# Kernel tuning notes

Measured on AMD Instinct MI355X. Metric: run time of the kernel, lower is better.

The kernel has to match this reference:

```python
import jax, jax.numpy as jnp
import numpy as np

NPOINT = 1024
RADII = (0.1, 0.2)
NSAMPLES = (16, 32)
IN_CH = 64
OUT = 256
EPS = 1e-5


def fps(pts, npoint):
    # pts: (N,3) -> (npoint,) int32 farthest-point-sampling indices (starts at index 0)
    N = pts.shape[0]
    def body(carry, _):
        dists, last = carry
        d = jnp.sum((pts - pts[last]) ** 2, axis=-1)
        dists = jnp.minimum(dists, d)
        nxt = jnp.argmax(dists).astype(jnp.int32)
        return (dists, nxt), last
    _, idx = jax.lax.scan(body, (jnp.full((N,), 1e10, pts.dtype), jnp.int32(0)), None, length=npoint)
    return idx


def ball_query(radius, k, xyz, new_xyz):
    # xyz (B,N,3), new_xyz (B,S,3) -> (B,S,k) int32; first k points within radius,
    # padded with the first in-range index (matches pointnet2 ball_query semantics;
    # each centroid is itself a point so at least one index is always in range).
    N = xyz.shape[1]
    d2 = jnp.sum((new_xyz[:, :, None, :] - xyz[:, None, :, :]) ** 2, axis=-1)  # (B,S,N)
    mask = d2 < radius * radius
    key = jnp.where(mask, jnp.arange(N, dtype=jnp.int32)[None, None, :], N)
    order = jnp.argsort(key, axis=-1)[..., :k]            # (B,S,k)
    sel_key = jnp.take_along_axis(key, order, axis=-1)
    valid = sel_key < N
    first = order[..., :1]
    return jnp.where(valid, order, first).astype(jnp.int32)


def gather(x, idx):
    # x (B,N,C), idx (B,...) -> (B,...,C)
    return jax.vmap(lambda f, i: f[i])(x, idx)


def bn_relu(x, gamma, beta):
    # BatchNorm (training-mode batch statistics) over all axes except channel (last), then ReLU
    axes = tuple(range(x.ndim - 1))
    mean = jnp.mean(x, axis=axes, keepdims=True)
    var = jnp.var(x, axis=axes, keepdims=True)
    return jax.nn.relu((x - mean) * jax.lax.rsqrt(var + EPS) * gamma + beta)


def _forward(xyz, feat, branch_params, fuse_params):
    idx_fps = jax.vmap(lambda p: fps(p, NPOINT))(xyz)     # (B,S)
    new_xyz = gather(xyz, idx_fps)                        # (B,S,3)
    outs = []
    for (r, k), (w1, g1, b1, w2, g2, b2) in zip(zip(RADII, NSAMPLES), branch_params):
        idx = ball_query(r, k, xyz, new_xyz)              # (B,S,k)
        rel = gather(xyz, idx) - new_xyz[:, :, None, :]   # (B,S,k,3)
        x = jnp.concatenate([rel, gather(feat, idx)], axis=-1)  # (B,S,k,Cin+3)
        x = bn_relu(jnp.einsum('bskc,oc->bsko', x, w1), g1, b1)
        x = bn_relu(jnp.einsum('bskc,oc->bsko', x, w2), g2, b2)
        outs.append(jnp.max(x, axis=2))                   # max-pool over nsample -> (B,S,OUT)
    x = jnp.concatenate(outs, axis=-1)                    # (B,S,len(RADII)*OUT)
    wf1, gf1, bf1, wf2, gf2, bf2 = fuse_params
    x = bn_relu(jnp.einsum('bsc,oc->bso', x, wf1), gf1, bf1)
    x = bn_relu(jnp.einsum('bsc,oc->bso', x, wf2), gf2, bf2)
    return new_xyz, x


def setup_inputs():
    key = jax.random.key(0)
    ks = jax.random.split(key, 16)
    B, N = 8, 4096
    xyz = jax.random.uniform(ks[0], (B, N, 3), dtype=jnp.float32)
    feat = jax.random.normal(ks[1], (B, N, IN_CH), dtype=jnp.float32)
    cin, mid = IN_CH + 3, OUT // 2
    def w(k, o, c):
        return jax.random.normal(k, (o, c), dtype=jnp.float32) * np.float32(1.0 / np.sqrt(c))
    inp = {"xyz": xyz, "feat": feat}
    i = 2
    for s in range(len(RADII)):
        inp[f"w1_{s}"] = w(ks[i], mid, cin); i += 1
        inp[f"g1_{s}"] = jnp.ones((mid,), jnp.float32)
        inp[f"b1_{s}"] = jnp.zeros((mid,), jnp.float32)
        inp[f"w2_{s}"] = w(ks[i], OUT, mid); i += 1
        inp[f"g2_{s}"] = jnp.ones((OUT,), jnp.float32)
        inp[f"b2_{s}"] = jnp.zeros((OUT,), jnp.float32)
    inp["wf1"] = w(ks[i], OUT, len(RADII) * OUT); i += 1
    inp["gf1"] = jnp.ones((OUT,), jnp.float32)
    inp["bf1"] = jnp.zeros((OUT,), jnp.float32)
    inp["wf2"] = w(ks[i], OUT, OUT)
    inp["gf2"] = jnp.ones((OUT,), jnp.float32)
    inp["bf2"] = jnp.zeros((OUT,), jnp.float32)
    return inp


def reference(xyz, feat, w1_0, g1_0, b1_0, w2_0, g2_0, b2_0,
              w1_1, g1_1, b1_1, w2_1, g2_1, b2_1,
              wf1, gf1, bf1, wf2, gf2, bf2):
    branch_params = [(w1_0, g1_0, b1_0, w2_0, g2_0, b2_0),
                     (w1_1, g1_1, b1_1, w2_1, g2_1, b2_1)]
    fuse_params = (wf1, gf1, bf1, wf2, gf2, bf2)
    return _forward(xyz, feat, branch_params, fuse_params)
```

## Files before the change

### kernel.cpp

```cpp
#include <hip/hip_runtime.h>


#define DEV __device__ __forceinline__

DEV float d2_nofma(float ax, float ay, float az, float bx, float by, float bz) {
#pragma clang fp contract(off)
  float dx = ax - bx, dy = ay - by, dz = az - bz;
  float s = dx * dx + dy * dy;
  return s + dz * dz;
}

DEV unsigned long long u64max(unsigned long long a, unsigned long long b) {
  return a > b ? a : b;
}

__global__ __launch_bounds__(512) void fps_kernel(
    const float* __restrict__ xyz, int* __restrict__ idx_out,
    float* __restrict__ nx_ws, float* __restrict__ nx_out) {
  __shared__ float sp[4096 * 3];
  __shared__ int hist[1024];
  __shared__ unsigned long long cand[2][8];
  const int b = blockIdx.x, t = threadIdx.x;
  const int w = t >> 6;
  const float* P = xyz + (size_t)b * 12288;
  float px[8], py[8], pz[8], dd[8];
#pragma unroll
  for (int j = 0; j < 8; j++) {
    int pi = t * 8 + j;
    float x = P[pi * 3], y = P[pi * 3 + 1], z = P[pi * 3 + 2];
    px[j] = x; py[j] = y; pz[j] = z; dd[j] = 1e10f;
    sp[pi * 3] = x; sp[pi * 3 + 1] = y; sp[pi * 3 + 2] = z;
  }
  __syncthreads();
  int last = 0;
  for (int it = 0; it < 1024; ++it) {
    if (t == 0) hist[it] = last;
    if (it == 1023) break;
    float lx = sp[last * 3], ly = sp[last * 3 + 1], lz = sp[last * 3 + 2];
    float bv = -1.0f;
    int bi = 0;
#pragma unroll
    for (int j = 0; j < 8; j++) {
      float d = d2_nofma(px[j], py[j], pz[j], lx, ly, lz);
      float nd = fminf(dd[j], d);
      dd[j] = nd;
      if (nd > bv) { bv = nd; bi = t * 8 + j; }
    }
    unsigned long long p =
        ((unsigned long long)__float_as_uint(bv) << 32) |
        (unsigned int)(4095 - bi);
#define DPP_MAX_STEP(CTRL)                                                  \
    {                                                                       \
      int lo_ = (int)(unsigned int)(p & 0xffffffffull);                     \
      int hi_ = (int)(unsigned int)(p >> 32);                               \
      int olo_ = __builtin_amdgcn_update_dpp(0, lo_, CTRL, 0xf, 0xf, false);\
      int ohi_ = __builtin_amdgcn_update_dpp(0, hi_, CTRL, 0xf, 0xf, false);\
      unsigned long long q_ =                                               \
          ((unsigned long long)(unsigned int)ohi_ << 32) |                  \
          (unsigned int)olo_;                                               \
      if (q_ > p) p = q_;                                                   \
    }
    DPP_MAX_STEP(0xB1);
    DPP_MAX_STEP(0x4E);
    DPP_MAX_STEP(0x124);
    DPP_MAX_STEP(0x128);
    DPP_MAX_STEP(0x142);
    DPP_MAX_STEP(0x143);
#undef DPP_MAX_STEP
    const int buf = it & 1;
    if ((t & 63) == 63) cand[buf][w] = p;
    __syncthreads();
    unsigned long long c0 = cand[buf][0], c1 = cand[buf][1];
    unsigned long long c2 = cand[buf][2], c3 = cand[buf][3];
    unsigned long long c4 = cand[buf][4], c5 = cand[buf][5];
    unsigned long long c6 = cand[buf][6], c7 = cand[buf][7];
    unsigned long long best =
        u64max(u64max(u64max(c0, c1), u64max(c2, c3)),
               u64max(u64max(c4, c5), u64max(c6, c7)));
    last = 4095 - (int)(unsigned int)(best & 0xffffffffull);
  }
  __syncthreads();
  for (int i = t; i < 1024; i += 512) {
    int id = hist[i];
    idx_out[(size_t)b * 1024 + i] = id;
    float x = sp[id * 3], y = sp[id * 3 + 1], z = sp[id * 3 + 2];
    size_t o = ((size_t)b * 1024 + i) * 3;
    nx_ws[o] = x; nx_ws[o + 1] = y; nx_ws[o + 2] = z;
    nx_out[o] = x; nx_out[o + 1] = y; nx_out[o + 2] = z;
  }
}

__global__ __launch_bounds__(256) void bq_kernel(
    const float* __restrict__ xyz, const float* __restrict__ nx,
    int* __restrict__ out0, int* __restrict__ out1) {
  const int wv = threadIdx.x >> 6, lane = threadIdx.x & 63;
  const int bs = blockIdx.x * 4 + wv;
  const int b = bs >> 10;
  const float* c = nx + (size_t)bs * 3;
  const float cx = c[0], cy = c[1], cz = c[2];
  const float* P = xyz + (size_t)b * 12288;
  const float rr0 = 0.1f * 0.1f, rr1 = 0.2f * 0.2f;
  int c0 = 0, c1 = 0, f0 = -1, f1 = -1;
  const unsigned long long below = (1ull << lane) - 1ull;
  for (int base = 0; base < 4096; base += 64) {
    int p = base + lane;
    float x = P[p * 3], y = P[p * 3 + 1], z = P[p * 3 + 2];
    float d2 = d2_nofma(cx, cy, cz, x, y, z);
    bool in0 = d2 < rr0, in1 = d2 < rr1;
    unsigned long long m0 = __ballot(in0), m1 = __ballot(in1);
    if (in0) {
      int slot = c0 + __popcll(m0 & below);
      if (slot < 16) out0[(size_t)bs * 16 + slot] = p;
    }
    if (in1) {
      int slot = c1 + __popcll(m1 & below);
      if (slot < 32) out1[(size_t)bs * 32 + slot] = p;
    }
    if (f0 < 0 && m0) f0 = base + __ffsll(m0) - 1;
    if (f1 < 0 && m1) f1 = base + __ffsll(m1) - 1;
    c0 += __popcll(m0);
    c1 += __popcll(m1);
    if (c0 >= 16 && c1 >= 32) break;
  }
  if (c0 < 16 && lane >= c0 && lane < 16) out0[(size_t)bs * 16 + lane] = f0;
  if (c1 < 32 && lane >= c1 && lane < 32) out1[(size_t)bs * 32 + lane] = f1;
}

template <int KS>
__global__ __launch_bounds__(256) void g1_kernel(
    const float* __restrict__ xyz, const float* __restrict__ feat,
    const float* __restrict__ nx, const int* __restrict__ idx,
    const float* __restrict__ w1, float* __restrict__ y1) {
  __shared__ float At[34][132];
  __shared__ float Bt[34][132];
  const int t = threadIdx.x;
  const int g0 = blockIdx.x * 128;
  const int tx = t & 15, ty = t >> 4;
  const int r = t >> 1, half = t & 1;
  const int g = g0 + r;
  const int bs = g / KS;
  const int b = bs >> 10;
  const int id = idx[g];
  const float* fp = feat + ((size_t)(b * 4096 + id)) * 64;
  float rel0 = 0, rel1 = 0, rel2 = 0;
  if (half == 0) {
    const float* cp = nx + (size_t)bs * 3;
    const float* pp = xyz + ((size_t)(b * 4096 + id)) * 3;
    rel0 = pp[0] - cp[0]; rel1 = pp[1] - cp[1]; rel2 = pp[2] - cp[2];
  }
  float acc[8][8];
#pragma unroll
  for (int i = 0; i < 8; i++)
#pragma unroll
    for (int j = 0; j < 8; j++) acc[i][j] = 0.f;

#pragma unroll
  for (int kc = 0; kc < 2; ++kc) {
    const int kb = kc * 34;
    const int kn = kc ? 33 : 34;
    {
      int c0 = half * 17;
      int cn = half ? (kn - 17) : 17;
      for (int u = 0; u < cn; u++) {
        int cabs = kb + c0 + u;
        float v;
        if (cabs < 3) v = (cabs == 0) ? rel0 : ((cabs == 1) ? rel1 : rel2);
        else v = fp[cabs - 3];
        At[c0 + u][r] = v;
      }
    }
    {
      int o = t >> 1;
      const float* wp = w1 + (size_t)o * 67;
      int c0 = half * 17;
      int cn = half ? (kn - 17) : 17;
      for (int u = 0; u < cn; u++) Bt[c0 + u][o] = wp[kb + c0 + u];
    }
    __syncthreads();
#pragma unroll 4
    for (int k = 0; k < kn; k++) {
      float4 a0 = *(const float4*)&At[k][ty * 4];
      float4 a1 = *(const float4*)&At[k][ty * 4 + 64];
      float4 b0 = *(const float4*)&Bt[k][tx * 4];
      float4 b1 = *(const float4*)&Bt[k][tx * 4 + 64];
      float av[8] = {a0.x, a0.y, a0.z, a0.w, a1.x, a1.y, a1.z, a1.w};
      float bv[8] = {b0.x, b0.y, b0.z, b0.w, b1.x, b1.y, b1.z, b1.w};
#pragma unroll
      for (int i = 0; i < 8; i++)
#pragma unroll
        for (int j = 0; j < 8; j++) acc[i][j] = fmaf(av[i], bv[j], acc[i][j]);
    }
    __syncthreads();
  }
#pragma unroll
  for (int i = 0; i < 8; i++) {
    int R = ty * 4 + (i & 3) + ((i >> 2) << 6);
    float4 s0 = {acc[i][0], acc[i][1], acc[i][2], acc[i][3]};
    float4 s1 = {acc[i][4], acc[i][5], acc[i][6], acc[i][7]};
    *(float4*)&y1[((size_t)(g0 + R)) * 128 + tx * 4] = s0;
    *(float4*)&y1[((size_t)(g0 + R)) * 128 + tx * 4 + 64] = s1;
  }
}

template <int KS>
__global__ __launch_bounds__(256, 2) void g2_kernel(
    const float* __restrict__ y1, const float* __restrict__ w2,
    const float* __restrict__ a1, const float* __restrict__ b1,
    float* __restrict__ pmin, float* __restrict__ pmax,
    float* __restrict__ statp) {
  __shared__ float At[32][132];
  __shared__ float Bt[32][260];
  const int t = threadIdx.x;
  const int g0 = blockIdx.x * 128;
  const int tx = t & 15, ty = t >> 4;
  float acc[8][16];
#pragma unroll
  for (int i = 0; i < 8; i++)
#pragma unroll
    for (int j = 0; j < 16; j++) acc[i][j] = 0.f;

  const int r = t >> 1, halfA = t & 1;
  const float* arow = y1 + (size_t)(g0 + r) * 128;
  for (int kc = 0; kc < 4; kc++) {
    {
      const int cb = kc * 32 + halfA * 16;
#pragma unroll
      for (int q = 0; q < 4; q++) {
        float4 v = *(const float4*)&arow[cb + q * 4];
        float vv[4] = {v.x, v.y, v.z, v.w};
#pragma unroll
        for (int e = 0; e < 4; e++) {
          int cabs = cb + q * 4 + e;
          float x = fmaxf(fmaf(a1[cabs], vv[e], b1[cabs]), 0.f);
          At[halfA * 16 + q * 4 + e][r] = x;
        }
      }
    }
    {
      const float* wrow = w2 + (size_t)t * 128 + kc * 32;
#pragma unroll
      for (int q = 0; q < 8; q++) {
        float4 w4 = *(const float4*)&wrow[q * 4];
        Bt[q * 4 + 0][t] = w4.x; Bt[q * 4 + 1][t] = w4.y;
        Bt[q * 4 + 2][t] = w4.z; Bt[q * 4 + 3][t] = w4.w;
      }
    }
    __syncthreads();
#pragma unroll 4
    for (int k = 0; k < 32; k++) {
      float4 a0 = *(const float4*)&At[k][ty * 4];
      float4 a1v = *(const float4*)&At[k][ty * 4 + 64];
      float4 b0 = *(const float4*)&Bt[k][tx * 4];
      float4 b1v = *(const float4*)&Bt[k][tx * 4 + 64];
      float4 b2v = *(const float4*)&Bt[k][tx * 4 + 128];
      float4 b3v = *(const float4*)&Bt[k][tx * 4 + 192];
      float av[8] = {a0.x, a0.y, a0.z, a0.w, a1v.x, a1v.y, a1v.z, a1v.w};
      float bv[16] = {b0.x, b0.y, b0.z, b0.w, b1v.x, b1v.y, b1v.z, b1v.w,
                      b2v.x, b2v.y, b2v.z, b2v.w, b3v.x, b3v.y, b3v.z, b3v.w};
#pragma unroll
      for (int i = 0; i < 8; i++)
#pragma unroll
        for (int j = 0; j < 16; j++) acc[i][j] = fmaf(av[i], bv[j], acc[i][j]);
    }
    __syncthreads();
  }

  float* red = &At[0][0];
  const int w = t >> 6;
  const bool wrsel = ((t & 48) == 0);
  const int NS = 128 / KS;

#pragma unroll
  for (int h = 0; h < 2; h++)
#pragma unroll
    for (int j = 0; j < 16; j++) {
      float x = acc[h * 4][j] + acc[h * 4 + 1][j] + acc[h * 4 + 2][j] + acc[h * 4 + 3][j];
      x += __shfl_xor(x, 16);
      x += __shfl_xor(x, 32);
      if (wrsel) red[(((w << 1) | h) << 8) + (tx << 2) + (j & 3) + ((j >> 2) << 6)] = x;
    }
  __syncthreads();
  float psum = 0;
  for (int e = 0; e < 8; e++) psum += red[(e << 8) + t];
  __syncthreads();
#pragma unroll
  for (int h = 0; h < 2; h++)
#pragma unroll
    for (int j = 0; j < 16; j++) {
      float x = acc[h * 4][j] * acc[h * 4][j];
      x = fmaf(acc[h * 4 + 1][j], acc[h * 4 + 1][j], x);
      x = fmaf(acc[h * 4 + 2][j], acc[h * 4 + 2][j], x);
      x = fmaf(acc[h * 4 + 3][j], acc[h * 4 + 3][j], x);
      x += __shfl_xor(x, 16);
      x += __shfl_xor(x, 32);
      if (wrsel) red[(((w << 1) | h) << 8) + (tx << 2) + (j & 3) + ((j >> 2) << 6)] = x;
    }
  __syncthreads();
  float psq = 0;
  for (int e = 0; e < 8; e++) psq += red[(e << 8) + t];
  statp[(size_t)blockIdx.x * 512 + t] = psum;
  statp[(size_t)blockIdx.x * 512 + 256 + t] = psq;
  __syncthreads();
#pragma unroll
  for (int h = 0; h < 2; h++)
#pragma unroll
    for (int j = 0; j < 16; j++) {
      float x = fminf(fminf(acc[h * 4][j], acc[h * 4 + 1][j]),
                      fminf(acc[h * 4 + 2][j], acc[h * 4 + 3][j]));
      x = fminf(x, __shfl_xor(x, 16));
      x = fminf(x, __shfl_xor(x, 32));
      if (wrsel) red[(((w << 1) | h) << 8) + (tx << 2) + (j & 3) + ((j >> 2) << 6)] = x;
    }
  __syncthreads();
  for (int cell = t; cell < NS * 256; cell += 256) {
    int sg = cell >> 8, col = cell & 255;
    float val;
    if (KS == 16) {
      int h = sg >> 2, ww = sg & 3;
      val = red[(((ww << 1) | h) << 8) + col];
    } else {
      int h = sg >> 1, w0 = (sg & 1) << 1;
      val = fminf(red[(((w0 << 1) | h) << 8) + col],
                  red[((((w0 + 1) << 1) | h) << 8) + col]);
    }
    pmin[(size_t)(blockIdx.x * NS + sg) * 256 + col] = val;
  }
  __syncthreads();
#pragma unroll
  for (int h = 0; h < 2; h++)
#pragma unroll
    for (int j = 0; j < 16; j++) {
      float x = fmaxf(fmaxf(acc[h * 4][j], acc[h * 4 + 1][j]),
                      fmaxf(acc[h * 4 + 2][j], acc[h * 4 + 3][j]));
      x = fmaxf(x, __shfl_xor(x, 16));
      x = fmaxf(x, __shfl_xor(x, 32));
      if (wrsel) red[(((w << 1) | h) << 8) + (tx << 2) + (j & 3) + ((j >> 2) << 6)] = x;
    }
  __syncthreads();
  for (int cell = t; cell < NS * 256; cell += 256) {
    int sg = cell >> 8, col = cell & 255;
    float val;
    if (KS == 16) {
      int h = sg >> 2, ww = sg & 3;
      val = red[(((ww << 1) | h) << 8) + col];
    } else {
      int h = sg >> 1, w0 = (sg & 1) << 1;
      val = fmaxf(red[(((w0 << 1) | h) << 8) + col],
                  red[((((w0 + 1) << 1) | h) << 8) + col]);
    }
    pmax[(size_t)(blockIdx.x * NS + sg) * 256 + col] = val;
  }
}

__global__ __launch_bounds__(256) void stats_partial(
    const float* __restrict__ x, float* __restrict__ statp, int M, int N) {
  const int nb = gridDim.x;
  const int rows = M / nb;
  const int r0 = blockIdx.x * rows;
  const int t = threadIdx.x;
  const int col = t & (N - 1);
  const int sub = t / N;
  const int nsub = 256 / N;
  float s = 0, q = 0;
  for (int rr = sub; rr < rows; rr += nsub) {
    float v = x[(size_t)(r0 + rr) * N + col];
    s += v;
    q = fmaf(v, v, q);
  }
  if (N == 256) {
    statp[(size_t)blockIdx.x * 512 + col] = s;
    statp[(size_t)blockIdx.x * 512 + 256 + col] = q;
  } else {
    __shared__ float ss[256], qq[256];
    ss[t] = s; qq[t] = q;
    __syncthreads();
    if (t < 128) {
      statp[(size_t)blockIdx.x * 256 + t] = ss[t] + ss[t + 128];
      statp[(size_t)blockIdx.x * 256 + 128 + t] = qq[t] + qq[t + 128];
    }
  }
}

__global__ __launch_bounds__(256) void finalize_affine(
    const float* __restrict__ statp, int nb, float invM,
    const float* __restrict__ gamma, const float* __restrict__ beta,
    float* __restrict__ aout, float* __restrict__ bout, int N) {
  const int c = blockIdx.x;
  const int t = threadIdx.x;
  float s = 0, q = 0;
  for (int i = t; i < nb; i += 256) {
    s += statp[(size_t)i * 2 * N + c];
    q += statp[(size_t)i * 2 * N + N + c];
  }
#pragma unroll
  for (int m = 1; m <= 32; m <<= 1) {
    s += __shfl_xor(s, m);
    q += __shfl_xor(q, m);
  }
  __shared__ float rs[4], rq[4];
  if ((t & 63) == 0) { rs[t >> 6] = s; rq[t >> 6] = q; }
  __syncthreads();
  if (t == 0) {
    s = rs[0] + rs[1] + rs[2] + rs[3];
    q = rq[0] + rq[1] + rq[2] + rq[3];
    float mean = s * invM;
    float var = q * invM - mean * mean;
    float ia = gamma[c] * rsqrtf(var + 1e-5f);
    aout[c] = ia;
    bout[c] = beta[c] - mean * ia;
  }
}

__global__ __launch_bounds__(256) void pool_concat(
    const float* __restrict__ pmin, const float* __restrict__ pmax,
    const float* __restrict__ a2, const float* __restrict__ b2,
    float* __restrict__ cat, int off) {
  int i = blockIdx.x * 256 + threadIdx.x;
  int row = i >> 8, c = i & 255;
  float a = a2[c];
  float v = (a > 0.f) ? pmax[i] : pmin[i];
  cat[(size_t)row * 512 + off + c] = fmaxf(fmaf(a, v, b2[c]), 0.f);
}

template <bool AFF>
__global__ __launch_bounds__(256) void f_kernel(
    const float* __restrict__ A, const float* __restrict__ W,
    const float* __restrict__ ain, const float* __restrict__ bin,
    float* __restrict__ Y, int K) {
  __shared__ float At[64][68];
  __shared__ float Bt[64][132];
  const int t = threadIdx.x, tx = t & 15, ty = t >> 4;
  const int g0 = blockIdx.x * 64, cb = blockIdx.y;
  float acc[4][8];
#pragma unroll
  for (int i = 0; i < 4; i++)
#pragma unroll
    for (int j = 0; j < 8; j++) acc[i][j] = 0.f;
  const int rA = t >> 2, qA = t & 3;
  const int oB = t >> 1, hB = t & 1;
  const float* arow = A + (size_t)(g0 + rA) * K + qA * 16;
  const float* wrow = W + (size_t)(cb * 128 + oB) * K + hB * 32;
  for (int kc = 0; kc < K; kc += 64) {
    {
#pragma unroll
      for (int q = 0; q < 4; q++) {
        float4 v = *(const float4*)&arow[kc + q * 4];
        float vv[4] = {v.x, v.y, v.z, v.w};
        if constexpr (AFF) {
          int c = kc + qA * 16 + q * 4;
#pragma unroll
          for (int e = 0; e < 4; e++)
            vv[e] = fmaxf(fmaf(ain[c + e], vv[e], bin[c + e]), 0.f);
        }
#pragma unroll
        for (int e = 0; e < 4; e++) At[qA * 16 + q * 4 + e][rA] = vv[e];
      }
    }
    {
#pragma unroll
      for (int q = 0; q < 8; q++) {
        float4 v = *(const float4*)&wrow[kc + q * 4];
        Bt[hB * 32 + q * 4 + 0][oB] = v.x;
        Bt[hB * 32 + q * 4 + 1][oB] = v.y;
        Bt[hB * 32 + q * 4 + 2][oB] = v.z;
        Bt[hB * 32 + q * 4 + 3][oB] = v.w;
      }
    }
    __syncthreads();
#pragma unroll 8
    for (int k = 0; k < 64; k++) {
      float4 a0 = *(const float4*)&At[k][ty * 4];
      float4 b0 = *(const float4*)&Bt[k][tx * 4];
      float4 b1 = *(const float4*)&Bt[k][tx * 4 + 64];
      float av[4] = {a0.x, a0.y, a0.z, a0.w};
      float bv[8] = {b0.x, b0.y, b0.z, b0.w, b1.x, b1.y, b1.z, b1.w};
#pragma unroll
      for (int i = 0; i < 4; i++)
#pragma unroll
        for (int j = 0; j < 8; j++) acc[i][j] = fmaf(av[i], bv[j], acc[i][j]);
    }
    __syncthreads();
  }
#pragma unroll
  for (int i = 0; i < 4; i++) {
    int R = g0 + ty * 4 + i;
    float4 s0 = {acc[i][0], acc[i][1], acc[i][2], acc[i][3]};
    float4 s1 = {acc[i][4], acc[i][5], acc[i][6], acc[i][7]};
    *(float4*)&Y[(size_t)R * 256 + cb * 128 + tx * 4] = s0;
    *(float4*)&Y[(size_t)R * 256 + cb * 128 + tx * 4 + 64] = s1;
  }
}

__global__ __launch_bounds__(256) void final_write(
    const float* __restrict__ y, const float* __restrict__ a,
    const float* __restrict__ b, float* __restrict__ out) {
  int i = blockIdx.x * 256 + threadIdx.x;
  int c = i & 255;
  out[i] = fmaxf(fmaf(a[c], y[i], b[c]), 0.f);
}

static const size_t OFF_IDXFPS = 0;
static const size_t OFF_NEWXYZ = 8192;
static const size_t OFF_IDX0 = 32768;
static const size_t OFF_IDX1 = 163840;
static const size_t OFF_Y1 = 425984;
static const size_t OFF_PMIN = 33980416;
static const size_t OFF_PMAX = 36077568;
static const size_t OFF_STATP = 38174720;
static const size_t OFF_CONCAT = 39223296;
static const size_t OFF_YF1 = 43417600;
static const size_t OFF_YF2 = 45514752;
static const size_t OFF_AFF = 47611904;

extern "C" void kernel_launch(void* const* d_in, const int* in_sizes, int n_in,
                              void* d_out, int out_size, void* d_ws,
                              size_t ws_size, hipStream_t stream) {
  const float* xyz = (const float*)d_in[0];
  const float* feat = (const float*)d_in[1];
  const float* w1_0 = (const float*)d_in[2];
  const float* g1_0 = (const float*)d_in[3];
  const float* b1_0 = (const float*)d_in[4];
  const float* w2_0 = (const float*)d_in[5];
  const float* g2_0 = (const float*)d_in[6];
  const float* b2_0 = (const float*)d_in[7];
  const float* w1_1 = (const float*)d_in[8];
  const float* g1_1 = (const float*)d_in[9];
  const float* b1_1 = (const float*)d_in[10];
  const float* w2_1 = (const float*)d_in[11];
  const float* g2_1 = (const float*)d_in[12];
  const float* b2_1 = (const float*)d_in[13];
  const float* wf1 = (const float*)d_in[14];
  const float* gf1 = (const float*)d_in[15];
  const float* bf1 = (const float*)d_in[16];
  const float* wf2 = (const float*)d_in[17];
  const float* gf2 = (const float*)d_in[18];
  const float* bf2 = (const float*)d_in[19];

  float* out = (float*)d_out;
  float* ws = (float*)d_ws;

  int* idxfps = (int*)(ws + OFF_IDXFPS);
  float* nx = ws + OFF_NEWXYZ;
  int* idx0 = (int*)(ws + OFF_IDX0);
  int* idx1 = (int*)(ws + OFF_IDX1);
  float* y1 = ws + OFF_Y1;
  float* pmin = ws + OFF_PMIN;
  float* pmax = ws + OFF_PMAX;
  float* statp = ws + OFF_STATP;
  float* cat = ws + OFF_CONCAT;
  float* yf1 = ws + OFF_YF1;
  float* yf2 = ws + OFF_YF2;
  float* a1 = ws + OFF_AFF;
  float* b1 = a1 + 128;
  float* a2 = b1 + 128;
  float* b2 = a2 + 256;
  float* af1 = b2 + 256;
  float* bf1a = af1 + 256;
  float* af2 = bf1a + 256;
  float* bf2a = af2 + 256;

  fps_kernel<<<8, 512, 0, stream>>>(xyz, idxfps, nx, out);
  bq_kernel<<<2048, 256, 0, stream>>>(xyz, nx, idx0, idx1);

  g1_kernel<16><<<1024, 256, 0, stream>>>(xyz, feat, nx, idx0, w1_0, y1);
  stats_partial<<<1024, 256, 0, stream>>>(y1, statp, 131072, 128);
  finalize_affine<<<128, 256, 0, stream>>>(statp, 1024, 1.f / 131072.f, g1_0, b1_0, a1, b1, 128);
  g2_kernel<16><<<1024, 256, 0, stream>>>(y1, w2_0, a1, b1, pmin, pmax, statp);
  finalize_affine<<<256, 256, 0, stream>>>(statp, 1024, 1.f / 131072.f, g2_0, b2_0, a2, b2, 256);
  pool_concat<<<8192, 256, 0, stream>>>(pmin, pmax, a2, b2, cat, 0);

  g1_kernel<32><<<2048, 256, 0, stream>>>(xyz, feat, nx, idx1, w1_1, y1);
  stats_partial<<<1024, 256, 0, stream>>>(y1, statp, 262144, 128);
  finalize_affine<<<128, 256, 0, stream>>>(statp, 1024, 1.f / 262144.f, g1_1, b1_1, a1, b1, 128);
  g2_kernel<32><<<2048, 256, 0, stream>>>(y1, w2_1, a1, b1, pmin, pmax, statp);
  finalize_affine<<<256, 256, 0, stream>>>(statp, 2048, 1.f / 262144.f, g2_1, b2_1, a2, b2, 256);
  pool_concat<<<8192, 256, 0, stream>>>(pmin, pmax, a2, b2, cat, 256);

  f_kernel<false><<<dim3(128, 2), 256, 0, stream>>>(cat, wf1, nullptr, nullptr, yf1, 512);
  stats_partial<<<1024, 256, 0, stream>>>(yf1, statp, 8192, 256);
  finalize_affine<<<256, 256, 0, stream>>>(statp, 1024, 1.f / 8192.f, gf1, bf1, af1, bf1a, 256);
  f_kernel<true><<<dim3(128, 2), 256, 0, stream>>>(yf1, wf2, af1, bf1a, yf2, 256);
  stats_partial<<<1024, 256, 0, stream>>>(yf2, statp, 8192, 256);
  finalize_affine<<<256, 256, 0, stream>>>(statp, 1024, 1.f / 8192.f, gf2, bf2, af2, bf2a, 256);
  final_write<<<8192, 256, 0, stream>>>(yf2, af2, bf2a, out + 24576);
}
```

Before: 1.453 ms.

## Fuse BatchNorm statistics into GEMM epilogues and simplify FPS argmax

The separate stats_partial passes are removed. Each g1 and f_kernel block now reduces per-column sums and sums of squares straight from its accumulator registers, using shuffles plus a shared-memory combine across waves. finalize_affine is launched with the matching new partial counts. This avoids re-reading the y1/yf1/yf2 activations from memory and saves four launches, in exchange for extra epilogue work and one more block barrier. Separately, the FPS local argmax becomes a max tree followed by a lowest-index select, which removes the branchy compare chain on the serial critical path.

```diff
diff --git a/kernel.cpp b/kernel.cpp
--- a/kernel.cpp
+++ b/kernel.cpp
@@ -37,15 +37,17 @@
     if (t == 0) hist[it] = last;
     if (it == 1023) break;
     float lx = sp[last * 3], ly = sp[last * 3 + 1], lz = sp[last * 3 + 2];
-    float bv = -1.0f;
-    int bi = 0;
 #pragma unroll
     for (int j = 0; j < 8; j++) {
       float d = d2_nofma(px[j], py[j], pz[j], lx, ly, lz);
-      float nd = fminf(dd[j], d);
-      dd[j] = nd;
-      if (nd > bv) { bv = nd; bi = t * 8 + j; }
-    }
+      dd[j] = fminf(dd[j], d);
+    }
+    float bv = fmaxf(fmaxf(fmaxf(dd[0], dd[1]), fmaxf(dd[2], dd[3])),
+                     fmaxf(fmaxf(dd[4], dd[5]), fmaxf(dd[6], dd[7])));
+    int bj = 7;
+#pragma unroll
+    for (int j = 6; j >= 0; j--) bj = (dd[j] == bv) ? j : bj;
+    int bi = t * 8 + bj;
     unsigned long long p =
         ((unsigned long long)__float_as_uint(bv) << 32) |
         (unsigned int)(4095 - bi);
@@ -130,7 +132,8 @@
 __global__ __launch_bounds__(256) void g1_kernel(
     const float* __restrict__ xyz, const float* __restrict__ feat,
     const float* __restrict__ nx, const int* __restrict__ idx,
-    const float* __restrict__ w1, float* __restrict__ y1) {
+    const float* __restrict__ w1, float* __restrict__ y1,
+    float* __restrict__ statp) {
   __shared__ float At[34][132];
   __shared__ float Bt[34][132];
   const int t = threadIdx.x;
@@ -200,6 +203,37 @@
     *(float4*)&y1[((size_t)(g0 + R)) * 128 + tx * 4] = s0;
     *(float4*)&y1[((size_t)(g0 + R)) * 128 + tx * 4 + 64] = s1;
   }
+  float s8[8], q8[8];
+#pragma unroll
+  for (int j = 0; j < 8; j++) {
+    float s = 0, q = 0;
+#pragma unroll
+    for (int i = 0; i < 8; i++) {
+      float v = acc[i][j];
+      s += v;
+      q = fmaf(v, v, q);
+    }
+    s += __shfl_xor(s, 16); s += __shfl_xor(s, 32);
+    q += __shfl_xor(q, 16); q += __shfl_xor(q, 32);
+    s8[j] = s; q8[j] = q;
+  }
+  float* red = &At[0][0];
+  const int wvx = t >> 6;
+  if ((t & 63) < 16) {
+#pragma unroll
+    for (int j = 0; j < 8; j++) {
+      int col = tx * 4 + (j & 3) + ((j >> 2) << 6);
+      red[wvx * 128 + col] = s8[j];
+      red[512 + wvx * 128 + col] = q8[j];
+    }
+  }
+  __syncthreads();
+  if (t < 128) {
+    float s = red[t] + red[128 + t] + red[256 + t] + red[384 + t];
+    float q = red[512 + t] + red[640 + t] + red[768 + t] + red[896 + t];
+    statp[(size_t)blockIdx.x * 256 + t] = s;
+    statp[(size_t)blockIdx.x * 256 + 128 + t] = q;
+  }
 }
 
 template <int KS>
@@ -352,35 +386,6 @@
   }
 }
 
-__global__ __launch_bounds__(256) void stats_partial(
-    const float* __restrict__ x, float* __restrict__ statp, int M, int N) {
-  const int nb = gridDim.x;
-  const int rows = M / nb;
-  const int r0 = blockIdx.x * rows;
-  const int t = threadIdx.x;
-  const int col = t & (N - 1);
-  const int sub = t / N;
-  const int nsub = 256 / N;
-  float s = 0, q = 0;
-  for (int rr = sub; rr < rows; rr += nsub) {
-    float v = x[(size_t)(r0 + rr) * N + col];
-    s += v;
-    q = fmaf(v, v, q);
-  }
-  if (N == 256) {
-    statp[(size_t)blockIdx.x * 512 + col] = s;
-    statp[(size_t)blockIdx.x * 512 + 256 + col] = q;
-  } else {
-    __shared__ float ss[256], qq[256];
-    ss[t] = s; qq[t] = q;
-    __syncthreads();
-    if (t < 128) {
-      statp[(size_t)blockIdx.x * 256 + t] = ss[t] + ss[t + 128];
-      statp[(size_t)blockIdx.x * 256 + 128 + t] = qq[t] + qq[t + 128];
-    }
-  }
-}
-
 __global__ __launch_bounds__(256) void finalize_affine(
     const float* __restrict__ statp, int nb, float invM,
     const float* __restrict__ gamma, const float* __restrict__ beta,
@@ -426,7 +431,7 @@
 __global__ __launch_bounds__(256) void f_kernel(
     const float* __restrict__ A, const float* __restrict__ W,
     const float* __restrict__ ain, const float* __restrict__ bin,
-    float* __restrict__ Y, int K) {
+    float* __restrict__ Y, int K, float* __restrict__ statp) {
   __shared__ float At[64][68];
   __shared__ float Bt[64][132];
   const int t = threadIdx.x, tx = t & 15, ty = t >> 4;
@@ -488,6 +493,37 @@
     float4 s1 = {acc[i][4], acc[i][5], acc[i][6], acc[i][7]};
     *(float4*)&Y[(size_t)R * 256 + cb * 128 + tx * 4] = s0;
     *(float4*)&Y[(size_t)R * 256 + cb * 128 + tx * 4 + 64] = s1;
+  }
+  float s8[8], q8[8];
+#pragma unroll
+  for (int j = 0; j < 8; j++) {
+    float s = 0, q = 0;
+#pragma unroll
+    for (int i = 0; i < 4; i++) {
+      float v = acc[i][j];
+      s += v;
+      q = fmaf(v, v, q);
+    }
+    s += __shfl_xor(s, 16); s += __shfl_xor(s, 32);
+    q += __shfl_xor(q, 16); q += __shfl_xor(q, 32);
+    s8[j] = s; q8[j] = q;
+  }
+  float* red = &At[0][0];
+  const int wvx = t >> 6;
+  if ((t & 63) < 16) {
+#pragma unroll
+    for (int j = 0; j < 8; j++) {
+      int col = tx * 4 + (j & 3) + ((j >> 2) << 6);
+      red[wvx * 128 + col] = s8[j];
+      red[512 + wvx * 128 + col] = q8[j];
+    }
+  }
+  __syncthreads();
+  if (t < 128) {
+    float s = red[t] + red[128 + t] + red[256 + t] + red[384 + t];
+    float q = red[512 + t] + red[640 + t] + red[768 + t] + red[896 + t];
+    statp[(size_t)blockIdx.x * 512 + cb * 128 + t] = s;
+    statp[(size_t)blockIdx.x * 512 + 256 + cb * 128 + t] = q;
   }
 }
 
@@ -562,25 +598,21 @@
   fps_kernel<<<8, 512, 0, stream>>>(xyz, idxfps, nx, out);
   bq_kernel<<<2048, 256, 0, stream>>>(xyz, nx, idx0, idx1);
 
-  g1_kernel<16><<<1024, 256, 0, stream>>>(xyz, feat, nx, idx0, w1_0, y1);
-  stats_partial<<<1024, 256, 0, stream>>>(y1, statp, 131072, 128);
+  g1_kernel<16><<<1024, 256, 0, stream>>>(xyz, feat, nx, idx0, w1_0, y1, statp);
   finalize_affine<<<128, 256, 0, stream>>>(statp, 1024, 1.f / 131072.f, g1_0, b1_0, a1, b1, 128);
   g2_kernel<16><<<1024, 256, 0, stream>>>(y1, w2_0, a1, b1, pmin, pmax, statp);
   finalize_affine<<<256, 256, 0, stream>>>(statp, 1024, 1.f / 131072.f, g2_0, b2_0, a2, b2, 256);
   pool_concat<<<8192, 256, 0, stream>>>(pmin, pmax, a2, b2, cat, 0);
 
-  g1_kernel<32><<<2048, 256, 0, stream>>>(xyz, feat, nx, idx1, w1_1, y1);
-  stats_partial<<<1024, 256, 0, stream>>>(y1, statp, 262144, 128);
-  finalize_affine<<<128, 256, 0, stream>>>(statp, 1024, 1.f / 262144.f, g1_1, b1_1, a1, b1, 128);
+  g1_kernel<32><<<2048, 256, 0, stream>>>(xyz, feat, nx, idx1, w1_1, y1, statp);
+  finalize_affine<<<128, 256, 0, stream>>>(statp, 2048, 1.f / 262144.f, g1_1, b1_1, a1, b1, 128);
   g2_kernel<32><<<2048, 256, 0, stream>>>(y1, w2_1, a1, b1, pmin, pmax, statp);
   finalize_affine<<<256, 256, 0, stream>>>(statp, 2048, 1.f / 262144.f, g2_1, b2_1, a2, b2, 256);
   pool_concat<<<8192, 256, 0, stream>>>(pmin, pmax, a2, b2, cat, 256);
 
-  f_kernel<false><<<dim3(128, 2), 256, 0, stream>>>(cat, wf1, nullptr, nullptr, yf1, 512);
-  stats_partial<<<1024, 256, 0, stream>>>(yf1, statp, 8192, 256);
-  finalize_affine<<<256, 256, 0, stream>>>(statp, 1024, 1.f / 8192.f, gf1, bf1, af1, bf1a, 256);
-  f_kernel<true><<<dim3(128, 2), 256, 0, stream>>>(yf1, wf2, af1, bf1a, yf2, 256);
-  stats_partial<<<1024, 256, 0, stream>>>(yf2, statp, 8192, 256);
-  finalize_affine<<<256, 256, 0, stream>>>(statp, 1024, 1.f / 8192.f, gf2, bf2, af2, bf2a, 256);
+  f_kernel<false><<<dim3(128, 2), 256, 0, stream>>>(cat, wf1, nullptr, nullptr, yf1, 512, statp);
+  finalize_affine<<<256, 256, 0, stream>>>(statp, 128, 1.f / 8192.f, gf1, bf1, af1, bf1a, 256);
+  f_kernel<true><<<dim3(128, 2), 256, 0, stream>>>(yf1, wf2, af1, bf1a, yf2, 256, statp);
+  finalize_affine<<<256, 256, 0, stream>>>(statp, 128, 1.f / 8192.f, gf2, bf2, af2, bf2a, 256);
   final_write<<<8192, 256, 0, stream>>>(yf2, af2, bf2a, out + 24576);
 }
```

Result: faster. 1.386 ms (-4.6%).
